# Kernel optimization log

Hardware: AMD Instinct MI355X
Metric: run time of the kernel (lower is better)

## Reference

```python
import jax, jax.numpy as jnp
import numpy as np

GROUPS = 4
GROUP_SIZE = 64
NORMED = True


def setup_inputs() -> dict:
    key = jax.random.key(0)
    k1, k2 = jax.random.split(key)
    x = jax.random.normal(k1, (2, 4096, 4096), dtype=jnp.float32)
    # weight: [groups*group_out, group_in] = [4096, 1024], init std 0.02 as in torch
    weight = jax.random.normal(k2, (4096, 1024), dtype=jnp.float32) * 0.02
    return {"x": x, "weight": weight}


def reference(x, weight):
    if NORMED:
        # F.rms_norm with eps=None uses finfo(dtype).eps
        eps = jnp.finfo(x.dtype).eps
        x = x * jax.lax.rsqrt(jnp.mean(x * x, axis=-1, keepdims=True) + eps)

    # bf16 cast of weight (matches torch `.bfloat16()`), quantize in flat chunks of GROUP_SIZE
    w = weight.astype(jnp.bfloat16)
    w_g = w.reshape(-1, GROUP_SIZE)
    scale = jnp.clip(jnp.mean(jnp.abs(w_g), axis=-1, keepdims=True), 1e-8, None)
    q = jnp.clip(jnp.round(w_g / scale), -1.0, 1.0)
    # STE: forward value is q*scale, gradient flows through w
    w_ternary = w + jax.lax.stop_gradient((q * scale).reshape(w.shape) - w)

    group_in = weight.shape[1]
    group_out = weight.shape[0] // GROUPS
    w_grouped = w_ternary.reshape(GROUPS, group_out, group_in)

    bsz = x.shape[:-1]
    x_g = x.reshape(bsz + (GROUPS, group_in))
    # block-diagonal grouped matmul; promote bf16 weight to x dtype (exact upcast)
    out = jnp.einsum('...gi,goi->...go', x_g, w_grouped.astype(x.dtype))
    return out.reshape(bsz + (GROUPS * group_out,))
```

## Files before the change

### kernel.cpp

```cpp
#include <hip/hip_runtime.h>
#include <hip/hip_bf16.h>
#include <stdint.h>

__device__ __forceinline__ unsigned short f2bf(float f) {
    __hip_bfloat16 h = __float2bfloat16(f);
    return *reinterpret_cast<unsigned short*>(&h);
}
__device__ __forceinline__ float bf2f(unsigned short u) {
    __hip_bfloat16 h = *reinterpret_cast<__hip_bfloat16*>(&u);
    return __bfloat162float(h);
}

typedef __attribute__((ext_vector_type(8))) short bf16x8;
typedef __attribute__((ext_vector_type(4))) float f32x4;

__device__ __forceinline__ void async16(const void* g, void* l) {
    __builtin_amdgcn_global_load_lds(
        (const __attribute__((address_space(1))) unsigned int*)g,
        (__attribute__((address_space(3))) unsigned int*)l,
        16, 0, 0);
}

__global__ __launch_bounds__(256) void quant_kernel(const float* __restrict__ W,
                                                    unsigned short* __restrict__ Wq) {
    int idx = blockIdx.x * 256 + threadIdx.x;
    float wf = W[idx];
    float wbf = bf2f(f2bf(wf));
    float a = fabsf(wbf);
    float s = a;
    #pragma unroll
    for (int off = 32; off; off >>= 1) s += __shfl_xor(s, off, 64);
    float mean = s * (1.0f / 64.0f);
    float sf = bf2f(f2bf(mean));
    sf = fmaxf(sf, 1.0011718e-08f);
    float quot = bf2f(f2bf(wbf / sf));
    float q = rintf(quot);
    q = fminf(1.0f, fmaxf(-1.0f, q));
    float qs = q * sf;
    float d  = bf2f(f2bf(qs - wbf));
    Wq[idx] = f2bf(wbf + d);
}

__global__ __launch_bounds__(256) void norm_kernel(const float* __restrict__ X,
                                                   unsigned short* __restrict__ Xb) {
    __shared__ float red[4];
    const long long row = blockIdx.x;
    const float4* xr = (const float4*)(X + row * 4096);
    const int t = threadIdx.x;
    float4 v[4];
    float ss = 0.f;
    #pragma unroll
    for (int i = 0; i < 4; ++i) {
        v[i] = xr[i * 256 + t];
        ss += v[i].x * v[i].x + v[i].y * v[i].y + v[i].z * v[i].z + v[i].w * v[i].w;
    }
    #pragma unroll
    for (int off = 32; off; off >>= 1) ss += __shfl_xor(ss, off, 64);
    if ((t & 63) == 0) red[t >> 6] = ss;
    __syncthreads();
    const float tot = red[0] + red[1] + red[2] + red[3];
    const float scale = 1.0f / sqrtf(tot * (1.0f / 4096.0f) + 1.1920928955078125e-07f);
    ushort4* ob = (ushort4*)(Xb + row * 4096);
    #pragma unroll
    for (int i = 0; i < 4; ++i) {
        ushort4 o;
        o.x = f2bf(v[i].x * scale);
        o.y = f2bf(v[i].y * scale);
        o.z = f2bf(v[i].z * scale);
        o.w = f2bf(v[i].w * scale);
        ob[i * 256 + t] = o;
    }
}

__global__ __launch_bounds__(512, 2) void gemm_kernel(const unsigned short* __restrict__ Xb,
                                                      const unsigned short* __restrict__ Wq,
                                                      float* __restrict__ Out) {
    __shared__ __attribute__((aligned(16))) unsigned short ls[65536];

    const int tid = threadIdx.x;
    const int lane = tid & 63;
    const int laneR = lane & 15;
    const int wv = tid >> 6;
    const int wr = wv >> 2;
    const int wc = wv & 3;

    const int bid = blockIdx.x;
    const int swz = (bid & 7) * 64 + (bid >> 3);
    const int bm0 = (swz & 31) * 256;
    const int bn0 = (swz >> 5) * 256;
    const int g = bn0 >> 10;

    const int srow = tid >> 3;
    const int cswz8 = (((tid & 7) ^ (srow & 7)) << 3);
    const unsigned short* aG = Xb + (long long)(bm0 + srow) * 4096 + g * 1024 + cswz8;
    const unsigned short* bG = Wq + (long long)(bn0 + srow) * 1024 + cswz8;

    const int col0 = (((lane >> 4) ^ (lane & 7)) << 3);
    const int col1 = col0 ^ 32;

    enum { A0 = 0, B0 = 16384, A1 = 32768, B1 = 49152 };

    const int aRow = (wr * 128 + laneR) * 64;
    const int bRow = (wc * 64 + laneR) * 64;

#define STAGE_A(base, kt, h) do { \
    async16(aG + ((long long)((h) * 128) * 4096 + (kt) * 64),      ls + (base) + (h) * 8192 + tid * 8); \
    async16(aG + ((long long)((h) * 128 + 64) * 4096 + (kt) * 64), ls + (base) + (h) * 8192 + 4096 + tid * 8); \
} while (0)
#define STAGE_B(base, kt, h) do { \
    async16(bG + ((long long)((h) * 128) * 1024 + (kt) * 64),      ls + (base) + (h) * 8192 + tid * 8); \
    async16(bG + ((long long)((h) * 128 + 64) * 1024 + (kt) * 64), ls + (base) + (h) * 8192 + 4096 + tid * 8); \
} while (0)
#define LD(off) (*(const bf16x8*)(ls + (off)))
#define MFMA_Q(MB, NB, bb) do { \
    _Pragma("unroll") \
    for (int mi = 0; mi < 4; ++mi) { \
        _Pragma("unroll") \
        for (int ni = 0; ni < 2; ++ni) { \
            acc[(MB) + mi][(NB) + ni] = __builtin_amdgcn_mfma_f32_16x16x32_bf16(a[mi][0], bb[ni][0], acc[(MB) + mi][(NB) + ni], 0, 0, 0); \
            acc[(MB) + mi][(NB) + ni] = __builtin_amdgcn_mfma_f32_16x16x32_bf16(a[mi][1], bb[ni][1], acc[(MB) + mi][(NB) + ni], 0, 0, 0); \
        } \
    } \
} while (0)
#define BAR() __builtin_amdgcn_s_barrier()
#define PRIO1() __builtin_amdgcn_s_setprio(1)
#define PRIO0() __builtin_amdgcn_s_setprio(0)

    f32x4 acc[8][4];
    #pragma unroll
    for (int i = 0; i < 8; ++i)
        #pragma unroll
        for (int j = 0; j < 4; ++j) acc[i][j] = (f32x4){0.f, 0.f, 0.f, 0.f};

    bf16x8 a[4][2], b[2][2], c[2][2];

    STAGE_A(A0, 0, 0); STAGE_A(A0, 0, 1);
    STAGE_B(B0, 0, 0); STAGE_B(B0, 0, 1);
    STAGE_B(B1, 1, 0); STAGE_B(B1, 1, 1);
    asm volatile("s_waitcnt vmcnt(4)" ::: "memory");
    BAR();

    #pragma unroll 1
    for (int it = 0; it < 8; ++it) {
        const int kt0 = it * 2, kt1 = kt0 + 1;
        const bool pf = (it < 7);

        #pragma unroll
        for (int ni = 0; ni < 2; ++ni) { b[ni][0] = LD(B0 + bRow + ni * 1024 + col0); b[ni][1] = LD(B0 + bRow + ni * 1024 + col1); }
        #pragma unroll
        for (int mi = 0; mi < 4; ++mi) { a[mi][0] = LD(A0 + aRow + mi * 1024 + col0); a[mi][1] = LD(A0 + aRow + mi * 1024 + col1); }
        STAGE_A(A1, kt1, 0);
        BAR(); PRIO1(); MFMA_Q(0, 0, b); PRIO0(); BAR();

        #pragma unroll
        for (int ni = 0; ni < 2; ++ni) { c[ni][0] = LD(B0 + bRow + (ni + 2) * 1024 + col0); c[ni][1] = LD(B0 + bRow + (ni + 2) * 1024 + col1); }
        STAGE_A(A1, kt1, 1);
        BAR(); PRIO1(); MFMA_Q(0, 2, c); PRIO0(); BAR();

        #pragma unroll
        for (int mi = 0; mi < 4; ++mi) { a[mi][0] = LD(A0 + aRow + 4096 + mi * 1024 + col0); a[mi][1] = LD(A0 + aRow + 4096 + mi * 1024 + col1); }
        if (pf) STAGE_B(B0, kt0 + 2, 0);
        BAR(); PRIO1(); MFMA_Q(4, 0, b); PRIO0(); BAR();

        if (pf) STAGE_B(B0, kt0 + 2, 1);
        BAR(); PRIO1(); MFMA_Q(4, 2, c); PRIO0();
        if (pf) { asm volatile("s_waitcnt vmcnt(4)" ::: "memory"); }
        else    { asm volatile("s_waitcnt vmcnt(0)" ::: "memory"); }
        BAR();

        #pragma unroll
        for (int ni = 0; ni < 2; ++ni) { b[ni][0] = LD(B1 + bRow + ni * 1024 + col0); b[ni][1] = LD(B1 + bRow + ni * 1024 + col1); }
        #pragma unroll
        for (int mi = 0; mi < 4; ++mi) { a[mi][0] = LD(A1 + aRow + mi * 1024 + col0); a[mi][1] = LD(A1 + aRow + mi * 1024 + col1); }
        if (pf) STAGE_A(A0, kt0 + 2, 0);
        BAR(); PRIO1(); MFMA_Q(0, 0, b); PRIO0(); BAR();

        #pragma unroll
        for (int ni = 0; ni < 2; ++ni) { c[ni][0] = LD(B1 + bRow + (ni + 2) * 1024 + col0); c[ni][1] = LD(B1 + bRow + (ni + 2) * 1024 + col1); }
        if (pf) STAGE_A(A0, kt0 + 2, 1);
        BAR(); PRIO1(); MFMA_Q(0, 2, c); PRIO0(); BAR();

        #pragma unroll
        for (int mi = 0; mi < 4; ++mi) { a[mi][0] = LD(A1 + aRow + 4096 + mi * 1024 + col0); a[mi][1] = LD(A1 + aRow + 4096 + mi * 1024 + col1); }
        if (pf) STAGE_B(B1, kt1 + 2, 0);
        BAR(); PRIO1(); MFMA_Q(4, 0, b); PRIO0(); BAR();

        if (pf) STAGE_B(B1, kt1 + 2, 1);
        BAR(); PRIO1(); MFMA_Q(4, 2, c); PRIO0();
        if (pf) { asm volatile("s_waitcnt vmcnt(4)" ::: "memory"); }
        BAR();
    }

    #pragma unroll
    for (int mi = 0; mi < 8; ++mi) {
        #pragma unroll
        for (int ni = 0; ni < 4; ++ni) {
            const int colo = bn0 + wc * 64 + ni * 16 + laneR;
            const int rowb = bm0 + wr * 128 + mi * 16 + (lane >> 4) * 4;
            #pragma unroll
            for (int r = 0; r < 4; ++r)
                Out[(long long)(rowb + r) * 4096 + colo] = acc[mi][ni][r];
        }
    }
#undef STAGE_A
#undef STAGE_B
#undef LD
#undef MFMA_Q
#undef BAR
#undef PRIO1
#undef PRIO0
}

extern "C" void kernel_launch(void* const* d_in, const int* in_sizes, int n_in,
                              void* d_out, int out_size, void* d_ws, size_t ws_size,
                              hipStream_t stream) {
    const float* x = (const float*)d_in[0];
    const float* w = (const float*)d_in[1];
    float* out = (float*)d_out;

    unsigned short* xb = (unsigned short*)d_ws;
    unsigned short* wq = xb + (size_t)8192 * 4096;

    quant_kernel<<<4096 * 1024 / 256, 256, 0, stream>>>(w, wq);
    norm_kernel<<<8192, 256, 0, stream>>>(x, xb);
    gemm_kernel<<<512, 512, 0, stream>>>(xb, wq, out);
}
```

Baseline: 322.0 us.

## Split A-fragment loads earlier, remap block tiles, use nontemporal output stores

Half of the second A sub-tile's LDS fragments are now loaded one phase earlier into a new register set, so the following phase issues fewer LDS reads before its MFMAs. The block-to-tile mapping changes so that consecutive blocks share the same M rows and walk across N tiles, which alters L2 reuse of the activation tiles. Output stores become nontemporal to avoid polluting cache. The changes add register pressure from the extra fragment buffer and may hurt weight reuse under the new tile order.

After: 330.8 us. 1.03x slower.

```diff
diff --git a/kernel.cpp b/kernel.cpp
--- a/kernel.cpp
+++ b/kernel.cpp
@@ -85,9 +85,8 @@
     const int wc = wv & 3;
 
     const int bid = blockIdx.x;
-    const int swz = (bid & 7) * 64 + (bid >> 3);
-    const int bm0 = (swz & 31) * 256;
-    const int bn0 = (swz >> 5) * 256;
+    const int bm0 = (bid >> 4) * 256;
+    const int bn0 = ((bid & 7) * 2 + ((bid >> 3) & 1)) * 256;
     const int g = bn0 >> 10;
 
     const int srow = tid >> 3;
@@ -112,14 +111,11 @@
     async16(bG + ((long long)((h) * 128 + 64) * 1024 + (kt) * 64), ls + (base) + (h) * 8192 + 4096 + tid * 8); \
 } while (0)
 #define LD(off) (*(const bf16x8*)(ls + (off)))
-#define MFMA_Q(MB, NB, bb) do { \
+#define MROW(AI, NB, FF, BB) do { \
     _Pragma("unroll") \
-    for (int mi = 0; mi < 4; ++mi) { \
-        _Pragma("unroll") \
-        for (int ni = 0; ni < 2; ++ni) { \
-            acc[(MB) + mi][(NB) + ni] = __builtin_amdgcn_mfma_f32_16x16x32_bf16(a[mi][0], bb[ni][0], acc[(MB) + mi][(NB) + ni], 0, 0, 0); \
-            acc[(MB) + mi][(NB) + ni] = __builtin_amdgcn_mfma_f32_16x16x32_bf16(a[mi][1], bb[ni][1], acc[(MB) + mi][(NB) + ni], 0, 0, 0); \
-        } \
+    for (int ni = 0; ni < 2; ++ni) { \
+        acc[AI][(NB) + ni] = __builtin_amdgcn_mfma_f32_16x16x32_bf16((FF)[0], (BB)[ni][0], acc[AI][(NB) + ni], 0, 0, 0); \
+        acc[AI][(NB) + ni] = __builtin_amdgcn_mfma_f32_16x16x32_bf16((FF)[1], (BB)[ni][1], acc[AI][(NB) + ni], 0, 0, 0); \
     } \
 } while (0)
 #define BAR() __builtin_amdgcn_s_barrier()
@@ -132,7 +128,7 @@
         #pragma unroll
         for (int j = 0; j < 4; ++j) acc[i][j] = (f32x4){0.f, 0.f, 0.f, 0.f};
 
-    bf16x8 a[4][2], b[2][2], c[2][2];
+    bf16x8 a[4][2], ah2[2][2], b[2][2], c[2][2];
 
     STAGE_A(A0, 0, 0); STAGE_A(A0, 0, 1);
     STAGE_B(B0, 0, 0); STAGE_B(B0, 0, 1);
@@ -142,7 +138,7 @@
 
     #pragma unroll 1
     for (int it = 0; it < 8; ++it) {
-        const int kt0 = it * 2, kt1 = kt0 + 1;
+        const int kt1 = it * 2 + 1;
         const bool pf = (it < 7);
 
         #pragma unroll
@@ -150,20 +146,30 @@
         #pragma unroll
         for (int mi = 0; mi < 4; ++mi) { a[mi][0] = LD(A0 + aRow + mi * 1024 + col0); a[mi][1] = LD(A0 + aRow + mi * 1024 + col1); }
         STAGE_A(A1, kt1, 0);
-        BAR(); PRIO1(); MFMA_Q(0, 0, b); PRIO0(); BAR();
+        BAR(); PRIO1();
+        MROW(0, 0, a[0], b); MROW(1, 0, a[1], b); MROW(2, 0, a[2], b); MROW(3, 0, a[3], b);
+        PRIO0(); BAR();
 
         #pragma unroll
         for (int ni = 0; ni < 2; ++ni) { c[ni][0] = LD(B0 + bRow + (ni + 2) * 1024 + col0); c[ni][1] = LD(B0 + bRow + (ni + 2) * 1024 + col1); }
+        #pragma unroll
+        for (int j = 0; j < 2; ++j) { ah2[j][0] = LD(A0 + aRow + 4096 + j * 1024 + col0); ah2[j][1] = LD(A0 + aRow + 4096 + j * 1024 + col1); }
         STAGE_A(A1, kt1, 1);
-        BAR(); PRIO1(); MFMA_Q(0, 2, c); PRIO0(); BAR();
-
-        #pragma unroll
-        for (int mi = 0; mi < 4; ++mi) { a[mi][0] = LD(A0 + aRow + 4096 + mi * 1024 + col0); a[mi][1] = LD(A0 + aRow + 4096 + mi * 1024 + col1); }
-        if (pf) STAGE_B(B0, kt0 + 2, 0);
-        BAR(); PRIO1(); MFMA_Q(4, 0, b); PRIO0(); BAR();
-
-        if (pf) STAGE_B(B0, kt0 + 2, 1);
-        BAR(); PRIO1(); MFMA_Q(4, 2, c); PRIO0();
+        BAR(); PRIO1();
+        MROW(0, 2, a[0], c); MROW(1, 2, a[1], c); MROW(2, 2, a[2], c); MROW(3, 2, a[3], c);
+        PRIO0(); BAR();
+
+        #pragma unroll
+        for (int j = 0; j < 2; ++j) { a[j][0] = LD(A0 + aRow + 4096 + (j + 2) * 1024 + col0); a[j][1] = LD(A0 + aRow + 4096 + (j + 2) * 1024 + col1); }
+        if (pf) STAGE_B(B0, kt1 + 1, 0);
+        BAR(); PRIO1();
+        MROW(4, 0, ah2[0], b); MROW(5, 0, ah2[1], b); MROW(6, 0, a[0], b); MROW(7, 0, a[1], b);
+        PRIO0(); BAR();
+
+        if (pf) STAGE_B(B0, kt1 + 1, 1);
+        BAR(); PRIO1();
+        MROW(4, 2, ah2[0], c); MROW(5, 2, ah2[1], c); MROW(6, 2, a[0], c); MROW(7, 2, a[1], c);
+        PRIO0();
         if (pf) { asm volatile("s_waitcnt vmcnt(4)" ::: "memory"); }
         else    { asm volatile("s_waitcnt vmcnt(0)" ::: "memory"); }
         BAR();
@@ -172,21 +178,31 @@
         for (int ni = 0; ni < 2; ++ni) { b[ni][0] = LD(B1 + bRow + ni * 1024 + col0); b[ni][1] = LD(B1 + bRow + ni * 1024 + col1); }
         #pragma unroll
         for (int mi = 0; mi < 4; ++mi) { a[mi][0] = LD(A1 + aRow + mi * 1024 + col0); a[mi][1] = LD(A1 + aRow + mi * 1024 + col1); }
-        if (pf) STAGE_A(A0, kt0 + 2, 0);
-        BAR(); PRIO1(); MFMA_Q(0, 0, b); PRIO0(); BAR();
+        if (pf) STAGE_A(A0, kt1 + 1, 0);
+        BAR(); PRIO1();
+        MROW(0, 0, a[0], b); MROW(1, 0, a[1], b); MROW(2, 0, a[2], b); MROW(3, 0, a[3], b);
+        PRIO0(); BAR();
 
         #pragma unroll
         for (int ni = 0; ni < 2; ++ni) { c[ni][0] = LD(B1 + bRow + (ni + 2) * 1024 + col0); c[ni][1] = LD(B1 + bRow + (ni + 2) * 1024 + col1); }
-        if (pf) STAGE_A(A0, kt0 + 2, 1);
-        BAR(); PRIO1(); MFMA_Q(0, 2, c); PRIO0(); BAR();
-
-        #pragma unroll
-        for (int mi = 0; mi < 4; ++mi) { a[mi][0] = LD(A1 + aRow + 4096 + mi * 1024 + col0); a[mi][1] = LD(A1 + aRow + 4096 + mi * 1024 + col1); }
+        #pragma unroll
+        for (int j = 0; j < 2; ++j) { ah2[j][0] = LD(A1 + aRow + 4096 + j * 1024 + col0); ah2[j][1] = LD(A1 + aRow + 4096 + j * 1024 + col1); }
+        if (pf) STAGE_A(A0, kt1 + 1, 1);
+        BAR(); PRIO1();
+        MROW(0, 2, a[0], c); MROW(1, 2, a[1], c); MROW(2, 2, a[2], c); MROW(3, 2, a[3], c);
+        PRIO0(); BAR();
+
+        #pragma unroll
+        for (int j = 0; j < 2; ++j) { a[j][0] = LD(A1 + aRow + 4096 + (j + 2) * 1024 + col0); a[j][1] = LD(A1 + aRow + 4096 + (j + 2) * 1024 + col1); }
         if (pf) STAGE_B(B1, kt1 + 2, 0);
-        BAR(); PRIO1(); MFMA_Q(4, 0, b); PRIO0(); BAR();
+        BAR(); PRIO1();
+        MROW(4, 0, ah2[0], b); MROW(5, 0, ah2[1], b); MROW(6, 0, a[0], b); MROW(7, 0, a[1], b);
+        PRIO0(); BAR();
 
         if (pf) STAGE_B(B1, kt1 + 2, 1);
-        BAR(); PRIO1(); MFMA_Q(4, 2, c); PRIO0();
+        BAR(); PRIO1();
+        MROW(4, 2, ah2[0], c); MROW(5, 2, ah2[1], c); MROW(6, 2, a[0], c); MROW(7, 2, a[1], c);
+        PRIO0();
         if (pf) { asm volatile("s_waitcnt vmcnt(4)" ::: "memory"); }
         BAR();
     }
@@ -199,13 +215,13 @@
             const int rowb = bm0 + wr * 128 + mi * 16 + (lane >> 4) * 4;
             #pragma unroll
             for (int r = 0; r < 4; ++r)
-                Out[(long long)(rowb + r) * 4096 + colo] = acc[mi][ni][r];
+                __builtin_nontemporal_store(acc[mi][ni][r], &Out[(long long)(rowb + r) * 4096 + colo]);
         }
     }
 #undef STAGE_A
 #undef STAGE_B
 #undef LD
-#undef MFMA_Q
+#undef MROW
 #undef BAR
 #undef PRIO1
 #undef PRIO0
```
